# Kernel tuning notes

Hardware: AMD Instinct MI355X
Metric: run time of the kernel (lower is better)

Reference implementation:

```python
import jax, jax.numpy as jnp
import numpy as np

N = 50000      # nodes
DEG = 16       # uniform degree -> E = N*DEG edges
E = N * DEG
D_IN = 256
D_OUT = 128


def setup_inputs() -> dict:
    key = jax.random.key(0)
    k_x, k_w, k_col = jax.random.split(key, 3)
    X = jax.random.normal(k_x, (N, D_IN), dtype=jnp.float32)
    weights = jax.random.normal(k_w, (D_IN, D_OUT), dtype=jnp.float32)
    # CSR adjacency: uniform degree for simplicity; row_pointers[i] = i*DEG
    row_pointers = (jnp.arange(N + 1, dtype=jnp.int32) * DEG)
    column_index = jax.random.randint(k_col, (E,), 0, N, dtype=jnp.int32)
    # Kernel tiling metadata (unused by the math; placeholders)
    n_blk = 3125
    blockPartition = jnp.ones((n_blk,), dtype=jnp.int32)
    edgeToColumn = jnp.zeros((E,), dtype=jnp.int32)
    edgeToRow = jnp.zeros((E,), dtype=jnp.int32)
    hybrid_type = jnp.zeros((n_blk,), dtype=jnp.int32)
    row_nzr = jnp.zeros((N,), dtype=jnp.int32)
    col_nzr = jnp.zeros((E,), dtype=jnp.int32)
    return {
        "X": X,
        "weights": weights,
        "row_pointers": row_pointers,
        "column_index": column_index,
        "blockPartition": blockPartition,
        "edgeToColumn": edgeToColumn,
        "edgeToRow": edgeToRow,
        "hybrid_type": hybrid_type,
        "row_nzr": row_nzr,
        "col_nzr": col_nzr,
    }


def reference(X, weights, row_pointers, column_index, blockPartition,
              edgeToColumn, edgeToRow, hybrid_type, row_nzr, col_nzr):
    # GCNConv (fixed=0): X' = X @ W, then block-sparse SpMM A @ X' where A is the
    # unweighted CSR adjacency (sum over in-neighbors).
    Xp = jnp.matmul(X, weights)  # [N, D_OUT]
    n = X.shape[0]
    e = column_index.shape[0]
    # Recover per-edge destination row from CSR row_pointers.
    edge_dst = jnp.searchsorted(row_pointers, jnp.arange(e, dtype=row_pointers.dtype),
                                side="right").astype(jnp.int32) - 1  # [E]
    gathered = Xp[column_index]  # [E, D_OUT] irregular gather
    out = jax.ops.segment_sum(gathered, edge_dst, num_segments=n)  # [N, D_OUT]
    return out
```

## Files before the change

kernel.cpp:

```cpp
#include <hip/hip_runtime.h>
#include <hip/hip_bf16.h>


constexpr int D_IN  = 256;
constexpr int D_OUT = 128;
constexpr int BM = 128;
constexpr int BK = 32;
constexpr int LDA = BK + 8;

using short8  = __attribute__((ext_vector_type(8))) short;
using float4v = __attribute__((ext_vector_type(4))) float;

__device__ inline ushort f2bf(float f) {
    unsigned u = __float_as_uint(f);
    u = (u + 0x7FFFu + ((u >> 16) & 1u)) >> 16;
    return (ushort)u;
}

__device__ inline uint pk2bf(float lo, float hi) {
    float2 t; t.x = lo; t.y = hi;
    __hip_bfloat162 b = __float22bfloat162_rn(t);
    return *(uint*)&b;
}

__global__ __launch_bounds__(256) void prep_wt(const float* __restrict__ W,
                                               ushort* __restrict__ WT) {
    int id = blockIdx.x * 256 + threadIdx.x;
    int nn = id >> 8;
    int k  = id & 255;
    WT[nn * 256 + k] = f2bf(W[k * D_OUT + nn]);
}

__global__ __launch_bounds__(256) void gemm_xw(const float* __restrict__ X,
                                               const ushort* __restrict__ WT,
                                               ushort* __restrict__ Xp, int n) {
    __shared__ ushort Asl[BM * LDA];
    __shared__ ushort Bsl[D_OUT * LDA];
    const int tid  = threadIdx.x;
    const int wave = tid >> 6;
    const int lane = tid & 63;
    const int quad = lane >> 4;
    const int l16  = lane & 15;
    const int row0 = blockIdx.x * BM;

    float4v acc[2][8];
#pragma unroll
    for (int i = 0; i < 2; ++i)
#pragma unroll
        for (int t = 0; t < 8; ++t) acc[i][t] = (float4v){0.f, 0.f, 0.f, 0.f};

    for (int k0 = 0; k0 < D_IN; k0 += BK) {
#pragma unroll
        for (int i = 0; i < 4; ++i) {
            int idx = i * 256 + tid;
            int r = idx >> 3;
            int c4 = idx & 7;
            int row = row0 + r; if (row > n - 1) row = n - 1;
            float4 v = *(const float4*)(X + (size_t)row * D_IN + k0 + c4 * 4);
            uint2 p;
            p.x = pk2bf(v.x, v.y);
            p.y = pk2bf(v.z, v.w);
            *(uint2*)(&Asl[r * LDA + c4 * 4]) = p;
        }
#pragma unroll
        for (int i = 0; i < 2; ++i) {
            int idx = i * 256 + tid;
            int r  = idx >> 2;
            int ch = idx & 3;
            short8 v = *(const short8*)(WT + r * 256 + k0 + ch * 8);
            *(short8*)(&Bsl[r * LDA + ch * 8]) = v;
        }
        __syncthreads();

        short8 a0 = *(const short8*)(&Asl[(wave * 32 +      l16) * LDA + quad * 8]);
        short8 a1 = *(const short8*)(&Asl[(wave * 32 + 16 + l16) * LDA + quad * 8]);
#pragma unroll
        for (int t = 0; t < 8; ++t) {
            short8 b = *(const short8*)(&Bsl[(t * 16 + l16) * LDA + quad * 8]);
            acc[0][t] = __builtin_amdgcn_mfma_f32_16x16x32_bf16(a0, b, acc[0][t], 0, 0, 0);
            acc[1][t] = __builtin_amdgcn_mfma_f32_16x16x32_bf16(a1, b, acc[1][t], 0, 0, 0);
        }
        __syncthreads();
    }

#pragma unroll
    for (int rt = 0; rt < 2; ++rt) {
#pragma unroll
        for (int t = 0; t < 8; ++t) {
#pragma unroll
            for (int r = 0; r < 4; ++r) {
                int row = row0 + wave * 32 + rt * 16 + quad * 4 + r;
                if (row < n)
                    Xp[(size_t)row * D_OUT + t * 16 + l16] = f2bf(acc[rt][t][r]);
            }
        }
    }
}

__global__ __launch_bounds__(256) void spmm_agg(const ushort* __restrict__ Xp,
                                                const int* __restrict__ rowp,
                                                const int* __restrict__ colx,
                                                float* __restrict__ out, int n) {
    const int node = blockIdx.x * 4 + (threadIdx.x >> 6);
    const int lane = threadIdx.x & 63;
    if (node >= n) return;
    const int e0 = rowp[node];
    const int e1 = rowp[node + 1];
    const ushort* src = Xp + lane * 2;
    float s0 = 0.f, s1 = 0.f;
    if (e1 - e0 == 16) {
        int c[16];
#pragma unroll
        for (int i = 0; i < 16; ++i) c[i] = colx[e0 + i];
        uint v[16];
#pragma unroll
        for (int i = 0; i < 16; ++i)
            v[i] = *(const uint*)(src + (size_t)c[i] * D_OUT);
#pragma unroll
        for (int i = 0; i < 16; ++i) {
            s0 += __uint_as_float(v[i] << 16);
            s1 += __uint_as_float(v[i] & 0xFFFF0000u);
        }
    } else {
        for (int e = e0; e < e1; ++e) {
            uint v = *(const uint*)(src + (size_t)colx[e] * D_OUT);
            s0 += __uint_as_float(v << 16);
            s1 += __uint_as_float(v & 0xFFFF0000u);
        }
    }
    union { float2 f; double d; } u;
    u.f.x = s0; u.f.y = s1;
    __builtin_nontemporal_store(u.d, (double*)(out + (size_t)node * D_OUT + lane * 2));
}

extern "C" void kernel_launch(void* const* d_in, const int* in_sizes, int n_in,
                              void* d_out, int out_size, void* d_ws, size_t ws_size,
                              hipStream_t stream) {
    const float* X    = (const float*)d_in[0];
    const float* W    = (const float*)d_in[1];
    const int*   rowp = (const int*)d_in[2];
    const int*   colx = (const int*)d_in[3];
    float*       out  = (float*)d_out;

    ushort* WT = (ushort*)d_ws;
    ushort* Xp = (ushort*)((char*)d_ws + 65536);

    const int n = in_sizes[0] / D_IN;

    prep_wt<<<dim3(128), dim3(256), 0, stream>>>(W, WT);
    gemm_xw<<<dim3((n + BM - 1) / BM), dim3(256), 0, stream>>>(X, WT, Xp, n);
    spmm_agg<<<dim3((n + 3) / 4), dim3(256), 0, stream>>>(Xp, rowp, colx, out, n);
}
```

Before: 146.8 us.

## Keep full W tile in LDS and load X fragments directly into registers

The GEMM now stages the whole bf16 transposed weight matrix (128x256, padded) into shared memory once per block. Each lane then reads its own X row fragments straight from global memory into MFMA operand registers, with no LDS staging for A. This removes the per-K-step barriers and the A round trip through LDS. The kernel is fully unrolled with launch bounds requesting 2 blocks, but the large LDS footprint (~76KB) and per-lane strided global reads may limit occupancy and coalescing.

```diff
diff --git a/kernel.cpp b/kernel.cpp
--- a/kernel.cpp
+++ b/kernel.cpp
@@ -4,9 +4,9 @@
 
 constexpr int D_IN  = 256;
 constexpr int D_OUT = 128;
-constexpr int BM = 128;
-constexpr int BK = 32;
-constexpr int LDA = BK + 8;
+constexpr int BM  = 128;
+constexpr int BK  = 32;
+constexpr int LDB = 296;
 
 using short8  = __attribute__((ext_vector_type(8))) short;
 using float4v = __attribute__((ext_vector_type(4))) float;
@@ -31,11 +31,10 @@
     WT[nn * 256 + k] = f2bf(W[k * D_OUT + nn]);
 }
 
-__global__ __launch_bounds__(256) void gemm_xw(const float* __restrict__ X,
-                                               const ushort* __restrict__ WT,
-                                               ushort* __restrict__ Xp, int n) {
-    __shared__ ushort Asl[BM * LDA];
-    __shared__ ushort Bsl[D_OUT * LDA];
+__global__ __launch_bounds__(256, 2) void gemm_xw(const float* __restrict__ X,
+                                                  const ushort* __restrict__ WT,
+                                                  ushort* __restrict__ Xp, int n) {
+    __shared__ ushort Bs[D_OUT * LDB];
     const int tid  = threadIdx.x;
     const int wave = tid >> 6;
     const int lane = tid & 63;
@@ -43,44 +42,44 @@
     const int l16  = lane & 15;
     const int row0 = blockIdx.x * BM;
 
+#pragma unroll
+    for (int i = 0; i < 16; ++i) {
+        int idx = i * 256 + tid;
+        int r   = idx >> 5;
+        int ch  = idx & 31;
+        short8 v = *(const short8*)(WT + r * 256 + ch * 8);
+        *(short8*)(&Bs[r * LDB + ch * 8]) = v;
+    }
+    __syncthreads();
+
+    int r0 = row0 + wave * 32 + l16;      if (r0 > n - 1) r0 = n - 1;
+    int r1 = row0 + wave * 32 + 16 + l16; if (r1 > n - 1) r1 = n - 1;
+    const float* xr0 = X + (size_t)r0 * D_IN + quad * 8;
+    const float* xr1 = X + (size_t)r1 * D_IN + quad * 8;
+
     float4v acc[2][8];
 #pragma unroll
     for (int i = 0; i < 2; ++i)
 #pragma unroll
         for (int t = 0; t < 8; ++t) acc[i][t] = (float4v){0.f, 0.f, 0.f, 0.f};
 
+#pragma unroll
     for (int k0 = 0; k0 < D_IN; k0 += BK) {
-#pragma unroll
-        for (int i = 0; i < 4; ++i) {
-            int idx = i * 256 + tid;
-            int r = idx >> 3;
-            int c4 = idx & 7;
-            int row = row0 + r; if (row > n - 1) row = n - 1;
-            float4 v = *(const float4*)(X + (size_t)row * D_IN + k0 + c4 * 4);
-            uint2 p;
-            p.x = pk2bf(v.x, v.y);
-            p.y = pk2bf(v.z, v.w);
-            *(uint2*)(&Asl[r * LDA + c4 * 4]) = p;
-        }
-#pragma unroll
-        for (int i = 0; i < 2; ++i) {
-            int idx = i * 256 + tid;
-            int r  = idx >> 2;
-            int ch = idx & 3;
-            short8 v = *(const short8*)(WT + r * 256 + k0 + ch * 8);
-            *(short8*)(&Bsl[r * LDA + ch * 8]) = v;
-        }
-        __syncthreads();
-
-        short8 a0 = *(const short8*)(&Asl[(wave * 32 +      l16) * LDA + quad * 8]);
-        short8 a1 = *(const short8*)(&Asl[(wave * 32 + 16 + l16) * LDA + quad * 8]);
+        float4 u0 = *(const float4*)(xr0 + k0);
+        float4 u1 = *(const float4*)(xr0 + k0 + 4);
+        float4 w0 = *(const float4*)(xr1 + k0);
+        float4 w1 = *(const float4*)(xr1 + k0 + 4);
+        union { short8 s; uint u[4]; } A0, A1;
+        A0.u[0] = pk2bf(u0.x, u0.y);  A0.u[1] = pk2bf(u0.z, u0.w);
+        A0.u[2] = pk2bf(u1.x, u1.y);  A0.u[3] = pk2bf(u1.z, u1.w);
+        A1.u[0] = pk2bf(w0.x, w0.y);  A1.u[1] = pk2bf(w0.z, w0.w);
+        A1.u[2] = pk2bf(w1.x, w1.y);  A1.u[3] = pk2bf(w1.z, w1.w);
 #pragma unroll
         for (int t = 0; t < 8; ++t) {
-            short8 b = *(const short8*)(&Bsl[(t * 16 + l16) * LDA + quad * 8]);
-            acc[0][t] = __builtin_amdgcn_mfma_f32_16x16x32_bf16(a0, b, acc[0][t], 0, 0, 0);
-            acc[1][t] = __builtin_amdgcn_mfma_f32_16x16x32_bf16(a1, b, acc[1][t], 0, 0, 0);
+            short8 b = *(const short8*)(&Bs[(t * 16 + l16) * LDB + k0 + quad * 8]);
+            acc[0][t] = __builtin_amdgcn_mfma_f32_16x16x32_bf16(A0.s, b, acc[0][t], 0, 0, 0);
+            acc[1][t] = __builtin_amdgcn_mfma_f32_16x16x32_bf16(A1.s, b, acc[1][t], 0, 0, 0);
         }
-        __syncthreads();
     }
 
 #pragma unroll
```

Result: no change. 146.3 us (-0.3%).
